# Performance work log

Hardware: AMD Instinct MI355X
Metric: run time of the kernel (lower is better)

Reference implementation:

```python
import jax, jax.numpy as jnp
import numpy as np


def setup_inputs() -> dict:
    key = jax.random.key(0)
    ks = jax.random.split(key, 16)
    B, T, H, E, V = 64, 512, 512, 512, 50257
    sc = 0.02  # weight init scale
    return {
        "enc_seq": jax.random.normal(ks[0], (B, T, H), jnp.float32),
        "enc_mask": jax.random.randint(ks[1], (B, T), 0, 2).astype(jnp.int32),
        "h0": jax.random.normal(ks[2], (1, B, H), jnp.float32),
        "c0": jax.random.normal(ks[3], (1, B, H), jnp.float32),
        "bos_id": 1,
        "eos_id": 2,
        "max_len": 28,
        "emb": jax.random.normal(ks[4], (V, E), jnp.float32) * sc,
        "W_h": jax.random.normal(ks[5], (H, H), jnp.float32) * sc,
        "W_s": jax.random.normal(ks[6], (H, H), jnp.float32) * sc,
        "v": jax.random.normal(ks[7], (H,), jnp.float32) * sc,
        "W_ih": jax.random.normal(ks[8], (4 * H, E + H), jnp.float32) * sc,
        "W_hh": jax.random.normal(ks[9], (4 * H, H), jnp.float32) * sc,
        "b_ih": jnp.zeros((4 * H,), jnp.float32),
        "b_hh": jnp.zeros((4 * H,), jnp.float32),
        "W_out": jax.random.normal(ks[10], (V, H), jnp.float32) * sc,
        "b_out": jnp.zeros((V,), jnp.float32),
    }


def reference(enc_seq, enc_mask, h0, c0, bos_id, eos_id, max_len,
              emb, W_h, W_s, v, W_ih, W_hh, b_ih, b_hh, W_out, b_out):
    B = enc_seq.shape[0]
    h = h0[0]  # [B, H]  (torch: transpose(0,1).squeeze(1))
    c = c0[0]
    # W_h(enc_seq) is loop-invariant; precompute once (same math as per-step recompute)
    Wh_enc = jnp.einsum('bth,kh->btk', enc_seq, W_h)  # [B, T, H]
    neg_inf = jnp.float32(-1e9)
    y0 = jnp.full((B,), bos_id, dtype=jnp.int32)

    def step(carry, _):
        h, c, y = carry
        e_t = emb[y]                                            # [B, E]
        s = h @ W_s.T                                           # [B, H]
        scores = jnp.einsum('bth,h->bt', jnp.tanh(Wh_enc + s[:, None, :]), v)
        scores = jnp.where(enc_mask == 0, neg_inf, scores)
        a = jax.nn.softmax(scores, axis=1)                      # [B, T]
        ctx = jnp.einsum('bt,bth->bh', a, enc_seq)              # [B, H]
        x = jnp.concatenate([e_t, ctx], axis=-1)                # [B, E+H]
        gates = x @ W_ih.T + h @ W_hh.T + b_ih + b_hh           # [B, 4H]
        i, f, g, o = jnp.split(gates, 4, axis=-1)               # torch gate order i,f,g,o
        c2 = jax.nn.sigmoid(f) * c + jax.nn.sigmoid(i) * jnp.tanh(g)
        h2 = jax.nn.sigmoid(o) * jnp.tanh(c2)
        # dropout is identity in eval mode (greedy decoding)
        logits = h2 @ W_out.T + b_out                           # [B, V]
        y2 = jnp.argmax(logits, axis=-1).astype(jnp.int32)
        return (h2, c2, y2), y2

    _, ys = jax.lax.scan(step, (h, c, y0), None, length=max_len - 1)
    return ys.T  # [B, max_len-1] greedy token ids
```

## Files before the change

### kernel.cpp

```cpp
#include <hip/hip_runtime.h>
#include <hip/hip_bf16.h>
#include <cmath>


#define TKK 16

typedef __attribute__((ext_vector_type(8))) short bf16x8;
typedef __attribute__((ext_vector_type(4))) float f32x4;

__device__ inline unsigned short bf16rn(float x) {
  unsigned int u = __float_as_uint(x);
  unsigned int r = u + 0x7fffu + ((u >> 16) & 1u);
  return (unsigned short)(r >> 16);
}
__device__ inline void split1(float x, unsigned short& h, unsigned short& l) {
  h = bf16rn(x);
  float hf = __uint_as_float(((unsigned int)h) << 16);
  l = bf16rn(x - hf);
}

__global__ __launch_bounds__(256) void gemm_tile(
    const float* __restrict__ A, int lda,
    const float* __restrict__ B, int ldb,
    float* __restrict__ C, int ldc,
    int Kchunk, long long c_zstride)
{
  __shared__ __align__(16) float At[TKK][68];
  __shared__ __align__(16) float Bt[TKK][132];
  const int tid = threadIdx.x;
  const int tx = tid & 15, ty = tid >> 4;
  const long long mbase = (long long)blockIdx.y * 64;
  const long long nbase = (long long)blockIdx.x * 128;
  const int kbase = blockIdx.z * Kchunk;
  const float* Ap = A + mbase * lda + kbase;
  const float* Bp = B + nbase * ldb + kbase;
  float acc[4][8];
#pragma unroll
  for (int i = 0; i < 4; i++)
#pragma unroll
    for (int j = 0; j < 8; j++) acc[i][j] = 0.f;

  const int lm = tid >> 2;
  const int lk = (tid & 3) << 2;
  for (int k0 = 0; k0 < Kchunk; k0 += TKK) {
    float4 av = *(const float4*)(Ap + (long long)lm * lda + k0 + lk);
    At[lk + 0][lm] = av.x; At[lk + 1][lm] = av.y;
    At[lk + 2][lm] = av.z; At[lk + 3][lm] = av.w;
#pragma unroll
    for (int r = 0; r < 2; r++) {
      int n = (tid + r * 256) >> 2;
      float4 bv = *(const float4*)(Bp + (long long)n * ldb + k0 + lk);
      Bt[lk + 0][n] = bv.x; Bt[lk + 1][n] = bv.y;
      Bt[lk + 2][n] = bv.z; Bt[lk + 3][n] = bv.w;
    }
    __syncthreads();
#pragma unroll
    for (int kk = 0; kk < TKK; ++kk) {
      float4 a4 = *(const float4*)&At[kk][ty * 4];
      float4 b0 = *(const float4*)&Bt[kk][tx * 4];
      float4 b1 = *(const float4*)&Bt[kk][64 + tx * 4];
      float as[4] = {a4.x, a4.y, a4.z, a4.w};
      float bs[8] = {b0.x, b0.y, b0.z, b0.w, b1.x, b1.y, b1.z, b1.w};
#pragma unroll
      for (int i = 0; i < 4; i++)
#pragma unroll
        for (int j = 0; j < 8; j++)
          acc[i][j] = fmaf(as[i], bs[j], acc[i][j]);
    }
    __syncthreads();
  }
  float* Cp = C + (long long)blockIdx.z * c_zstride;
#pragma unroll
  for (int i = 0; i < 4; i++) {
    long long m = mbase + ty * 4 + i;
    float4 v0, v1;
    v0.x = acc[i][0]; v0.y = acc[i][1]; v0.z = acc[i][2]; v0.w = acc[i][3];
    v1.x = acc[i][4]; v1.y = acc[i][5]; v1.z = acc[i][6]; v1.w = acc[i][7];
    *(float4*)(Cp + m * ldc + nbase + tx * 4) = v0;
    *(float4*)(Cp + m * ldc + nbase + 64 + tx * 4) = v1;
  }
}

__global__ __launch_bounds__(256) void wcat_kernel(
    const float* __restrict__ W_ih, const float* __restrict__ W_hh,
    float* __restrict__ wcat)
{
  long long fi = (long long)blockIdx.x * 256 + threadIdx.x;
  if (fi >= 2048LL * 1536 / 4) return;
  int k = (int)(fi / 384);
  int c = (int)(fi % 384) * 4;
  float4 v;
  if (c < 1024) v = *(const float4*)(W_ih + (long long)k * 1024 + c);
  else          v = *(const float4*)(W_hh + (long long)k * 512 + (c - 1024));
  *(float4*)(wcat + fi * 4) = v;
}

__global__ __launch_bounds__(256) void wcat_split_kernel(
    const float* __restrict__ W_ih, const float* __restrict__ W_hh,
    unsigned short* __restrict__ whi, unsigned short* __restrict__ wlo)
{
  long long fi = (long long)blockIdx.x * 256 + threadIdx.x;
  if (fi >= 2048LL * 1536 / 4) return;
  int k = (int)(fi / 384);
  int c = (int)(fi % 384) * 4;
  float4 v;
  if (c < 1024) v = *(const float4*)(W_ih + (long long)k * 1024 + c);
  else          v = *(const float4*)(W_hh + (long long)k * 512 + (c - 1024));
  long long e = fi * 4;
  float xs[4] = {v.x, v.y, v.z, v.w};
#pragma unroll
  for (int q = 0; q < 4; q++) {
    unsigned short h, l; split1(xs[q], h, l);
    whi[e + q] = h; wlo[e + q] = l;
  }
}

__global__ __launch_bounds__(256) void split_kernel(
    const float* __restrict__ src, unsigned short* __restrict__ hi,
    unsigned short* __restrict__ lo, long long n)
{
  long long i = (long long)blockIdx.x * 256 + threadIdx.x;
  long long stride = (long long)gridDim.x * 256;
  for (long long e = i * 4; e < n; e += stride * 4) {
    float4 v = *(const float4*)(src + e);
    float xs[4] = {v.x, v.y, v.z, v.w};
#pragma unroll
    for (int q = 0; q < 4; q++) {
      unsigned short h, l; split1(xs[q], h, l);
      hi[e + q] = h; lo[e + q] = l;
    }
  }
}

__global__ __launch_bounds__(256) void init_kernel(
    const float* __restrict__ h0, const float* __restrict__ c0,
    const int* __restrict__ bos,
    float* __restrict__ h, float* __restrict__ c, int* __restrict__ y,
    unsigned short* __restrict__ h_hi, unsigned short* __restrict__ h_lo)
{
  int i = blockIdx.x * 256 + threadIdx.x;
  if (i < 64 * 512) {
    float hv = h0[i];
    h[i] = hv; c[i] = c0[i];
    unsigned short hh, hl; split1(hv, hh, hl);
    h_hi[i] = hh; h_lo[i] = hl;
  }
  if (i < 64) y[i] = bos[0];
}

__global__ __launch_bounds__(256) void scores_kernel(
    const float* __restrict__ whenc,
    const float* __restrict__ spart, int np,
    const float* __restrict__ vvec,
    const int* __restrict__ mask,
    float* __restrict__ scores)
{
  const int b = blockIdx.x, tc = blockIdx.y, tid = threadIdx.x;
  __shared__ __align__(16) float sS[512];
  __shared__ __align__(16) float sV[512];
  for (int i = tid; i < 512; i += 256) {
    float s = 0.f;
    for (int p = 0; p < np; ++p) s += spart[(long long)p * 64 * 512 + b * 512 + i];
    sS[i] = s;
    sV[i] = vvec[i];
  }
  __syncthreads();
  const int wave = tid >> 6, lane = tid & 63;
  const int t0 = tc * 128 + wave * 32;
  for (int tt = 0; tt < 32; ++tt) {
    int t = t0 + tt;
    const float* row = whenc + ((long long)b * 512 + t) * 512;
    float p = 0.f;
#pragma unroll
    for (int u = 0; u < 2; ++u) {
      int hb = u * 256 + lane * 4;
      float4 w = *(const float4*)(row + hb);
      float4 s4 = *(const float4*)&sS[hb];
      float4 v4 = *(const float4*)&sV[hb];
      p = fmaf(v4.x, tanhf(w.x + s4.x), p);
      p = fmaf(v4.y, tanhf(w.y + s4.y), p);
      p = fmaf(v4.z, tanhf(w.z + s4.z), p);
      p = fmaf(v4.w, tanhf(w.w + s4.w), p);
    }
#pragma unroll
    for (int off = 32; off; off >>= 1) p += __shfl_xor(p, off);
    if (lane == 0)
      scores[b * 512 + t] = mask[b * 512 + t] ? p : -1e9f;
  }
}

__global__ __launch_bounds__(256) void ctx_kernel(
    const float* __restrict__ scores,
    const float* __restrict__ enc,
    float* __restrict__ ctxp)
{
  const int b = blockIdx.x, tc = blockIdx.y, tid = threadIdx.x;
  __shared__ float sc[512];
  __shared__ float red[256];
  float l0 = scores[b * 512 + tid];
  float l1 = scores[b * 512 + 256 + tid];
  red[tid] = fmaxf(l0, l1);
  __syncthreads();
  for (int s = 128; s > 0; s >>= 1) {
    if (tid < s) red[tid] = fmaxf(red[tid], red[tid + s]);
    __syncthreads();
  }
  float mx = red[0];
  __syncthreads();
  float e0 = expf(l0 - mx), e1 = expf(l1 - mx);
  sc[tid] = e0; sc[tid + 256] = e1;
  red[tid] = e0 + e1;
  __syncthreads();
  for (int s = 128; s > 0; s >>= 1) {
    if (tid < s) red[tid] += red[tid + s];
    __syncthreads();
  }
  float inv = 1.f / red[0];
  float a0 = 0.f, a1 = 0.f;
  for (int u = 0; u < 128; ++u) {
    int t = tc * 128 + u;
    float w = sc[t] * inv;
    const float* row = enc + ((long long)b * 512 + t) * 512;
    float2 e = *(const float2*)(row + tid * 2);
    a0 = fmaf(w, e.x, a0);
    a1 = fmaf(w, e.y, a1);
  }
  float2 o; o.x = a0; o.y = a1;
  *(float2*)(ctxp + ((long long)(b * 4 + tc)) * 512 + tid * 2) = o;
}

__global__ __launch_bounds__(256) void xbuild_kernel(
    const float* __restrict__ emb, const int* __restrict__ y,
    const float* __restrict__ ctxp, const float* __restrict__ h,
    float* __restrict__ xf,
    unsigned short* __restrict__ xhi, unsigned short* __restrict__ xlo)
{
  const int b = blockIdx.x, tid = threadIdx.x;
  const int yb = y[b];
  for (int i = tid; i < 1536; i += 256) {
    float val;
    if (i < 512) {
      val = emb[(long long)yb * 512 + i];
    } else if (i < 1024) {
      int hh = i - 512;
      val = ctxp[(b * 4 + 0) * 512 + hh] + ctxp[(b * 4 + 1) * 512 + hh]
          + ctxp[(b * 4 + 2) * 512 + hh] + ctxp[(b * 4 + 3) * 512 + hh];
    } else {
      val = h[b * 512 + (i - 1024)];
    }
    if (xf) xf[b * 1536 + i] = val;
    if (xhi) {
      unsigned short hh2, ll2; split1(val, hh2, ll2);
      xhi[b * 1536 + i] = hh2; xlo[b * 1536 + i] = ll2;
    }
  }
}

__global__ __launch_bounds__(512) void lstm_kernel(
    const float* __restrict__ gpart, int ngparts,
    const float* __restrict__ b_ih, const float* __restrict__ b_hh,
    float* __restrict__ h, float* __restrict__ c,
    unsigned short* __restrict__ h_hi, unsigned short* __restrict__ h_lo)
{
  const int b = blockIdx.x, hc = threadIdx.x;
  float g[4];
#pragma unroll
  for (int q = 0; q < 4; q++) {
    int k = q * 512 + hc;
    float s = b_ih[k] + b_hh[k];
    for (int p = 0; p < ngparts; ++p)
      s += gpart[((long long)p * 64 + b) * 2048 + k];
    g[q] = s;
  }
  float ig = 1.f / (1.f + expf(-g[0]));
  float fg = 1.f / (1.f + expf(-g[1]));
  float gg = tanhf(g[2]);
  float og = 1.f / (1.f + expf(-g[3]));
  float c2 = fg * c[b * 512 + hc] + ig * gg;
  float h2 = og * tanhf(c2);
  c[b * 512 + hc] = c2;
  h[b * 512 + hc] = h2;
  if (h_hi) {
    unsigned short hh, hl; split1(h2, hh, hl);
    h_hi[b * 512 + hc] = hh; h_lo[b * 512 + hc] = hl;
  }
}

__global__ __launch_bounds__(256) void mfma_gemm(
    const unsigned short* __restrict__ Ahi, const unsigned short* __restrict__ Alo,
    const unsigned short* __restrict__ Bhi, const unsigned short* __restrict__ Blo,
    float* __restrict__ C, int K, int N)
{
  const int tid = threadIdx.x;
  const int w = tid >> 6, l = tid & 63;
  const int arow = blockIdx.y * 64 + w * 16 + (l & 15);
  const int koff = (l >> 4) * 8;
  const int nbase = blockIdx.x * 64;
  f32x4 acc[4];
#pragma unroll
  for (int cf = 0; cf < 4; ++cf) acc[cf] = (f32x4){0.f, 0.f, 0.f, 0.f};

  for (int k0 = 0; k0 < K; k0 += 32) {
    bf16x8 ahi = *(const bf16x8*)(Ahi + (size_t)arow * K + k0 + koff);
    bf16x8 alo = *(const bf16x8*)(Alo + (size_t)arow * K + k0 + koff);
#pragma unroll
    for (int cf = 0; cf < 4; ++cf) {
      int col = nbase + cf * 16 + (l & 15);
      bf16x8 bhi = *(const bf16x8*)(Bhi + (size_t)col * K + k0 + koff);
      bf16x8 blo = *(const bf16x8*)(Blo + (size_t)col * K + k0 + koff);
      acc[cf] = __builtin_amdgcn_mfma_f32_16x16x32_bf16(ahi, bhi, acc[cf], 0, 0, 0);
      acc[cf] = __builtin_amdgcn_mfma_f32_16x16x32_bf16(ahi, blo, acc[cf], 0, 0, 0);
      acc[cf] = __builtin_amdgcn_mfma_f32_16x16x32_bf16(alo, bhi, acc[cf], 0, 0, 0);
    }
  }
#pragma unroll
  for (int cf = 0; cf < 4; ++cf) {
    int col = nbase + cf * 16 + (l & 15);
#pragma unroll
    for (int j = 0; j < 4; ++j) {
      int rowc = blockIdx.y * 64 + w * 16 + (l >> 4) * 4 + j;
      C[(size_t)rowc * N + col] = acc[cf][j];
    }
  }
}

__global__ __launch_bounds__(256) void mfma_logits(
    const unsigned short* __restrict__ Ahi, const unsigned short* __restrict__ Alo,
    const unsigned short* __restrict__ Bhi, const unsigned short* __restrict__ Blo,
    const float* __restrict__ bias, int V, int K,
    float* __restrict__ pval, int* __restrict__ pidx, int nvc)
{
  const int tid = threadIdx.x;
  const int w = tid >> 6, l = tid & 63;
  const int arow = w * 16 + (l & 15);
  const int koff = (l >> 4) * 8;
  const int nbase = blockIdx.x * 64;
  const bf16x8 bz = {0, 0, 0, 0, 0, 0, 0, 0};
  f32x4 acc[4];
#pragma unroll
  for (int cf = 0; cf < 4; ++cf) acc[cf] = (f32x4){0.f, 0.f, 0.f, 0.f};

  for (int k0 = 0; k0 < K; k0 += 32) {
    bf16x8 ahi = *(const bf16x8*)(Ahi + (size_t)arow * K + k0 + koff);
    bf16x8 alo = *(const bf16x8*)(Alo + (size_t)arow * K + k0 + koff);
#pragma unroll
    for (int cf = 0; cf < 4; ++cf) {
      int col = nbase + cf * 16 + (l & 15);
      bf16x8 bhi = bz, blo = bz;
      if (col < V) {
        bhi = *(const bf16x8*)(Bhi + (size_t)col * K + k0 + koff);
        blo = *(const bf16x8*)(Blo + (size_t)col * K + k0 + koff);
      }
      acc[cf] = __builtin_amdgcn_mfma_f32_16x16x32_bf16(ahi, bhi, acc[cf], 0, 0, 0);
      acc[cf] = __builtin_amdgcn_mfma_f32_16x16x32_bf16(ahi, blo, acc[cf], 0, 0, 0);
      acc[cf] = __builtin_amdgcn_mfma_f32_16x16x32_bf16(alo, bhi, acc[cf], 0, 0, 0);
    }
  }
#pragma unroll
  for (int j = 0; j < 4; ++j) {
    float bv = -INFINITY; int bi = 0x7fffffff;
#pragma unroll
    for (int cf = 0; cf < 4; ++cf) {
      int col = nbase + cf * 16 + (l & 15);
      if (col < V) {
        float v = acc[cf][j] + bias[col];
        if (v > bv) { bv = v; bi = col; }
      }
    }
#pragma unroll
    for (int off = 1; off <= 8; off <<= 1) {
      float ov = __shfl_xor(bv, off);
      int oi = __shfl_xor(bi, off);
      if (ov > bv || (ov == bv && oi < bi)) { bv = ov; bi = oi; }
    }
    if ((l & 15) == 0) {
      int b = w * 16 + (l >> 4) * 4 + j;
      pval[b * nvc + blockIdx.x] = bv;
      pidx[b * nvc + blockIdx.x] = bi;
    }
  }
}

__global__ __launch_bounds__(256) void logits_kernel(
    const float* __restrict__ A,
    const float* __restrict__ W,
    const float* __restrict__ bias,
    int V, float* __restrict__ pval, int* __restrict__ pidx, int nvc)
{
  __shared__ __align__(16) float At[TKK][68];
  __shared__ __align__(16) float Bt[TKK][132];
  __shared__ float lv[64][16];
  __shared__ int   li[64][16];
  const int tid = threadIdx.x;
  const int tx = tid & 15, ty = tid >> 4;
  const int nbase = blockIdx.x * 128;
  float acc[4][8];
#pragma unroll
  for (int i = 0; i < 4; i++)
#pragma unroll
    for (int j = 0; j < 8; j++) acc[i][j] = 0.f;
  const int lm = tid >> 2;
  const int lk = (tid & 3) << 2;
  for (int k0 = 0; k0 < 512; k0 += TKK) {
    float4 av = *(const float4*)(A + lm * 512 + k0 + lk);
    At[lk + 0][lm] = av.x; At[lk + 1][lm] = av.y;
    At[lk + 2][lm] = av.z; At[lk + 3][lm] = av.w;
#pragma unroll
    for (int r = 0; r < 2; r++) {
      int n = (tid + r * 256) >> 2;
      int ng = nbase + n;
      float4 bv = make_float4(0.f, 0.f, 0.f, 0.f);
      if (ng < V) bv = *(const float4*)(W + (long long)ng * 512 + k0 + lk);
      Bt[lk + 0][n] = bv.x; Bt[lk + 1][n] = bv.y;
      Bt[lk + 2][n] = bv.z; Bt[lk + 3][n] = bv.w;
    }
    __syncthreads();
#pragma unroll
    for (int kk = 0; kk < TKK; ++kk) {
      float4 a4 = *(const float4*)&At[kk][ty * 4];
      float4 b0 = *(const float4*)&Bt[kk][tx * 4];
      float4 b1 = *(const float4*)&Bt[kk][64 + tx * 4];
      float as[4] = {a4.x, a4.y, a4.z, a4.w};
      float bs[8] = {b0.x, b0.y, b0.z, b0.w, b1.x, b1.y, b1.z, b1.w};
#pragma unroll
      for (int i = 0; i < 4; i++)
#pragma unroll
        for (int j = 0; j < 8; j++)
          acc[i][j] = fmaf(as[i], bs[j], acc[i][j]);
    }
    __syncthreads();
  }
#pragma unroll
  for (int i = 0; i < 4; i++) {
    float bv_ = -INFINITY; int bi_ = 0x7fffffff;
#pragma unroll
    for (int j = 0; j < 8; j++) {
      int vg = (j < 4) ? (nbase + tx * 4 + j) : (nbase + 64 + tx * 4 + (j - 4));
      if (vg < V) {
        float val = acc[i][j] + bias[vg];
        if (val > bv_ || (val == bv_ && vg < bi_)) { bv_ = val; bi_ = vg; }
      }
    }
    lv[ty * 4 + i][tx] = bv_; li[ty * 4 + i][tx] = bi_;
  }
  __syncthreads();
  if (tid < 64) {
    float bv_ = -INFINITY; int bi_ = 0x7fffffff;
#pragma unroll
    for (int t = 0; t < 16; t++) {
      if (lv[tid][t] > bv_ || (lv[tid][t] == bv_ && li[tid][t] < bi_)) {
        bv_ = lv[tid][t]; bi_ = li[tid][t];
      }
    }
    pval[tid * nvc + blockIdx.x] = bv_;
    pidx[tid * nvc + blockIdx.x] = bi_;
  }
}

__global__ __launch_bounds__(64) void argfinal_kernel(
    const float* __restrict__ pval, const int* __restrict__ pidx, int nvc,
    int* __restrict__ y, int* __restrict__ out, int step, int steps)
{
  const int b = blockIdx.x, lane = threadIdx.x;
  float bv = -INFINITY; int bi = 0x7fffffff;
  for (int ci = lane; ci < nvc; ci += 64) {
    float v = pval[b * nvc + ci];
    int ix = pidx[b * nvc + ci];
    if (v > bv || (v == bv && ix < bi)) { bv = v; bi = ix; }
  }
#pragma unroll
  for (int off = 32; off; off >>= 1) {
    float ov = __shfl_xor(bv, off);
    int oi = __shfl_xor(bi, off);
    if (ov > bv || (ov == bv && oi < bi)) { bv = ov; bi = oi; }
  }
  if (lane == 0) { y[b] = bi; out[b * steps + step] = bi; }
}

extern "C" void kernel_launch(void* const* d_in, const int* in_sizes, int n_in,
                              void* d_out, int out_size, void* d_ws, size_t ws_size,
                              hipStream_t stream) {
  const float* enc_seq = (const float*)d_in[0];
  const int*   enc_mask = (const int*)d_in[1];
  const float* h0 = (const float*)d_in[2];
  const float* c0 = (const float*)d_in[3];
  const int*   bos = (const int*)d_in[4];
  const float* emb = (const float*)d_in[7];
  const float* W_h = (const float*)d_in[8];
  const float* W_s = (const float*)d_in[9];
  const float* vvec = (const float*)d_in[10];
  const float* W_ih = (const float*)d_in[11];
  const float* W_hh = (const float*)d_in[12];
  const float* b_ih = (const float*)d_in[13];
  const float* b_hh = (const float*)d_in[14];
  const float* W_out = (const float*)d_in[15];
  const float* b_out = (const float*)d_in[16];

  const int B = 64, T = 512, H = 512;
  const int Vn = in_sizes[15] / 512;
  const int steps = out_size / B;
  int* out = (int*)d_out;

  float* ws = (float*)d_ws;
  size_t off = 0;
  auto alloc = [&](size_t n) { float* p = ws + off; off += (n + 15) & ~(size_t)15; return p; };

  const size_t NEW_NEED = 200ull << 20;
  if (ws_size >= NEW_NEED) {
    const int NVC = (Vn + 63) / 64;
    float* whenc  = alloc((size_t)B * T * H);
    float* sbuf   = alloc((size_t)B * T);
    float* spartf = alloc((size_t)B * H);
    float* ctxp   = alloc((size_t)B * 4 * H);
    float* gbuf   = alloc((size_t)B * 2048);
    float* hbuf   = alloc((size_t)B * H);
    float* cbuf   = alloc((size_t)B * H);
    float* pval   = alloc((size_t)B * NVC);
    int*   pidx   = (int*)alloc((size_t)B * NVC);
    int*   ybuf   = (int*)alloc(B);
    unsigned short* h_hi  = (unsigned short*)alloc((size_t)B * H / 2);
    unsigned short* h_lo  = (unsigned short*)alloc((size_t)B * H / 2);
    unsigned short* x_hi  = (unsigned short*)alloc((size_t)B * 1536 / 2);
    unsigned short* x_lo  = (unsigned short*)alloc((size_t)B * 1536 / 2);
    unsigned short* ws_hi = (unsigned short*)alloc(512ull * 512 / 2);
    unsigned short* ws_lo = (unsigned short*)alloc(512ull * 512 / 2);
    unsigned short* wc_hi = (unsigned short*)alloc(2048ull * 1536 / 2);
    unsigned short* wc_lo = (unsigned short*)alloc(2048ull * 1536 / 2);
    unsigned short* wo_hi = (unsigned short*)alloc((size_t)Vn * 512 / 2);
    unsigned short* wo_lo = (unsigned short*)alloc((size_t)Vn * 512 / 2);

    init_kernel<<<128, 256, 0, stream>>>(h0, c0, bos, hbuf, cbuf, ybuf, h_hi, h_lo);
    wcat_split_kernel<<<3072, 256, 0, stream>>>(W_ih, W_hh, wc_hi, wc_lo);
    split_kernel<<<256, 256, 0, stream>>>(W_s, ws_hi, ws_lo, 512ll * 512);
    split_kernel<<<4096, 256, 0, stream>>>(W_out, wo_hi, wo_lo, (long long)Vn * 512);

    gemm_tile<<<dim3(4, 512, 1), 256, 0, stream>>>(
        enc_seq, 512, W_h, 512, whenc, 512, 512, 0);

    for (int step = 0; step < steps; ++step) {
      mfma_gemm<<<dim3(8, 1), 256, 0, stream>>>(h_hi, h_lo, ws_hi, ws_lo,
                                                spartf, 512, 512);
      scores_kernel<<<dim3(64, 4), 256, 0, stream>>>(whenc, spartf, 1, vvec,
                                                     enc_mask, sbuf);
      ctx_kernel<<<dim3(64, 4), 256, 0, stream>>>(sbuf, enc_seq, ctxp);
      xbuild_kernel<<<64, 256, 0, stream>>>(emb, ybuf, ctxp, hbuf,
                                            nullptr, x_hi, x_lo);
      mfma_gemm<<<dim3(32, 1), 256, 0, stream>>>(x_hi, x_lo, wc_hi, wc_lo,
                                                 gbuf, 1536, 2048);
      lstm_kernel<<<64, 512, 0, stream>>>(gbuf, 1, b_ih, b_hh, hbuf, cbuf,
                                          h_hi, h_lo);
      mfma_logits<<<NVC, 256, 0, stream>>>(h_hi, h_lo, wo_hi, wo_lo, b_out,
                                           Vn, 512, pval, pidx, NVC);
      argfinal_kernel<<<64, 64, 0, stream>>>(pval, pidx, NVC, ybuf, out,
                                             step, steps);
    }
  } else {
    const int NVC = (Vn + 127) / 128;
    float* whenc  = alloc((size_t)B * T * H);
    float* sbuf   = alloc((size_t)B * T);
    float* spart  = alloc(4ull * B * H);
    float* ctxp   = alloc((size_t)B * 4 * H);
    float* xbuf   = alloc((size_t)B * 1536);
    float* gpart  = alloc(3ull * B * 2048);
    float* wcat   = alloc(2048ull * 1536);
    float* hbuf   = alloc((size_t)B * H);
    float* cbuf   = alloc((size_t)B * H);
    float* pval   = alloc((size_t)B * NVC);
    int*   ybuf   = (int*)alloc(B);
    int*   pidx   = (int*)alloc((size_t)B * NVC);
    unsigned short* h_hi = (unsigned short*)alloc((size_t)B * H / 2);
    unsigned short* h_lo = (unsigned short*)alloc((size_t)B * H / 2);

    init_kernel<<<128, 256, 0, stream>>>(h0, c0, bos, hbuf, cbuf, ybuf, h_hi, h_lo);
    wcat_kernel<<<3072, 256, 0, stream>>>(W_ih, W_hh, wcat);
    gemm_tile<<<dim3(4, 512, 1), 256, 0, stream>>>(
        enc_seq, 512, W_h, 512, whenc, 512, 512, 0);

    for (int step = 0; step < steps; ++step) {
      gemm_tile<<<dim3(4, 1, 4), 256, 0, stream>>>(
          hbuf, 512, W_s, 512, spart, 512, 128, (long long)B * H);
      scores_kernel<<<dim3(64, 4), 256, 0, stream>>>(whenc, spart, 4, vvec,
                                                     enc_mask, sbuf);
      ctx_kernel<<<dim3(64, 4), 256, 0, stream>>>(sbuf, enc_seq, ctxp);
      xbuild_kernel<<<64, 256, 0, stream>>>(emb, ybuf, ctxp, hbuf,
                                            xbuf, nullptr, nullptr);
      gemm_tile<<<dim3(16, 1, 3), 256, 0, stream>>>(
          xbuf, 1536, wcat, 1536, gpart, 2048, 512, (long long)B * 2048);
      lstm_kernel<<<64, 512, 0, stream>>>(gpart, 3, b_ih, b_hh, hbuf, cbuf,
                                          nullptr, nullptr);
      logits_kernel<<<NVC, 256, 0, stream>>>(hbuf, W_out, b_out, Vn,
                                             pval, pidx, NVC);
      argfinal_kernel<<<64, 64, 0, stream>>>(pval, pidx, NVC, ybuf, out,
                                             step, steps);
    }
  }
}
```

Measured before the change: 6.973 ms.

## Unify MFMA path, add on-the-fly W_out split fallback, fast tanh, prefetch

The fallback path is removed. The low-workspace case now uses an MFMA logits kernel that splits fp32 W_out into bf16 hi/lo pairs on the fly, so it no longer needs the scalar FMA tiled GEMM. The attention scores kernel replaces tanhf with an exp-plus-reciprocal approximation, trading some accuracy for cheaper transcendentals. mfma_gemm now register double-buffers its global loads to overlap them with MFMA work, and leftover partial-sum reductions and null checks are dropped. The on-the-fly split truncates the hi part instead of rounding it, so results can differ slightly from the precomputed path.

```diff
diff --git a/kernel.cpp b/kernel.cpp
--- a/kernel.cpp
+++ b/kernel.cpp
@@ -17,6 +17,19 @@
   h = bf16rn(x);
   float hf = __uint_as_float(((unsigned int)h) << 16);
   l = bf16rn(x - hf);
+}
+__device__ inline void split_tr(float x, short& h, short& l) {
+  unsigned int u = __float_as_uint(x);
+  h = (short)(u >> 16);
+  float hf = __uint_as_float(u & 0xffff0000u);
+  float d = x - hf;
+  unsigned int ud = __float_as_uint(d);
+  unsigned int r = ud + 0x7fffu + ((ud >> 16) & 1u);
+  l = (short)(r >> 16);
+}
+__device__ inline float tanh_fast(float x) {
+  float e = __expf(2.f * x);
+  return 1.f - 2.f * __builtin_amdgcn_rcpf(e + 1.f);
 }
 
 __global__ __launch_bounds__(256) void gemm_tile(
@@ -81,20 +94,6 @@
   }
 }
 
-__global__ __launch_bounds__(256) void wcat_kernel(
-    const float* __restrict__ W_ih, const float* __restrict__ W_hh,
-    float* __restrict__ wcat)
-{
-  long long fi = (long long)blockIdx.x * 256 + threadIdx.x;
-  if (fi >= 2048LL * 1536 / 4) return;
-  int k = (int)(fi / 384);
-  int c = (int)(fi % 384) * 4;
-  float4 v;
-  if (c < 1024) v = *(const float4*)(W_ih + (long long)k * 1024 + c);
-  else          v = *(const float4*)(W_hh + (long long)k * 512 + (c - 1024));
-  *(float4*)(wcat + fi * 4) = v;
-}
-
 __global__ __launch_bounds__(256) void wcat_split_kernel(
     const float* __restrict__ W_ih, const float* __restrict__ W_hh,
     unsigned short* __restrict__ whi, unsigned short* __restrict__ wlo)
@@ -150,7 +149,7 @@
 
 __global__ __launch_bounds__(256) void scores_kernel(
     const float* __restrict__ whenc,
-    const float* __restrict__ spart, int np,
+    const float* __restrict__ sarr,
     const float* __restrict__ vvec,
     const int* __restrict__ mask,
     float* __restrict__ scores)
@@ -159,9 +158,7 @@
   __shared__ __align__(16) float sS[512];
   __shared__ __align__(16) float sV[512];
   for (int i = tid; i < 512; i += 256) {
-    float s = 0.f;
-    for (int p = 0; p < np; ++p) s += spart[(long long)p * 64 * 512 + b * 512 + i];
-    sS[i] = s;
+    sS[i] = sarr[b * 512 + i];
     sV[i] = vvec[i];
   }
   __syncthreads();
@@ -177,10 +174,10 @@
       float4 w = *(const float4*)(row + hb);
       float4 s4 = *(const float4*)&sS[hb];
       float4 v4 = *(const float4*)&sV[hb];
-      p = fmaf(v4.x, tanhf(w.x + s4.x), p);
-      p = fmaf(v4.y, tanhf(w.y + s4.y), p);
-      p = fmaf(v4.z, tanhf(w.z + s4.z), p);
-      p = fmaf(v4.w, tanhf(w.w + s4.w), p);
+      p = fmaf(v4.x, tanh_fast(w.x + s4.x), p);
+      p = fmaf(v4.y, tanh_fast(w.y + s4.y), p);
+      p = fmaf(v4.z, tanh_fast(w.z + s4.z), p);
+      p = fmaf(v4.w, tanh_fast(w.w + s4.w), p);
     }
 #pragma unroll
     for (int off = 32; off; off >>= 1) p += __shfl_xor(p, off);
@@ -232,7 +229,6 @@
 __global__ __launch_bounds__(256) void xbuild_kernel(
     const float* __restrict__ emb, const int* __restrict__ y,
     const float* __restrict__ ctxp, const float* __restrict__ h,
-    float* __restrict__ xf,
     unsigned short* __restrict__ xhi, unsigned short* __restrict__ xlo)
 {
   const int b = blockIdx.x, tid = threadIdx.x;
@@ -248,16 +244,13 @@
     } else {
       val = h[b * 512 + (i - 1024)];
     }
-    if (xf) xf[b * 1536 + i] = val;
-    if (xhi) {
-      unsigned short hh2, ll2; split1(val, hh2, ll2);
-      xhi[b * 1536 + i] = hh2; xlo[b * 1536 + i] = ll2;
-    }
+    unsigned short hh2, ll2; split1(val, hh2, ll2);
+    xhi[b * 1536 + i] = hh2; xlo[b * 1536 + i] = ll2;
   }
 }
 
 __global__ __launch_bounds__(512) void lstm_kernel(
-    const float* __restrict__ gpart, int ngparts,
+    const float* __restrict__ gates,
     const float* __restrict__ b_ih, const float* __restrict__ b_hh,
     float* __restrict__ h, float* __restrict__ c,
     unsigned short* __restrict__ h_hi, unsigned short* __restrict__ h_lo)
@@ -267,10 +260,7 @@
 #pragma unroll
   for (int q = 0; q < 4; q++) {
     int k = q * 512 + hc;
-    float s = b_ih[k] + b_hh[k];
-    for (int p = 0; p < ngparts; ++p)
-      s += gpart[((long long)p * 64 + b) * 2048 + k];
-    g[q] = s;
+    g[q] = b_ih[k] + b_hh[k] + gates[(long long)b * 2048 + k];
   }
   float ig = 1.f / (1.f + expf(-g[0]));
   float fg = 1.f / (1.f + expf(-g[1]));
@@ -280,10 +270,8 @@
   float h2 = og * tanhf(c2);
   c[b * 512 + hc] = c2;
   h[b * 512 + hc] = h2;
-  if (h_hi) {
-    unsigned short hh, hl; split1(h2, hh, hl);
-    h_hi[b * 512 + hc] = hh; h_lo[b * 512 + hc] = hl;
-  }
+  unsigned short hh, hl; split1(h2, hh, hl);
+  h_hi[b * 512 + hc] = hh; h_lo[b * 512 + hc] = hl;
 }
 
 __global__ __launch_bounds__(256) void mfma_gemm(
@@ -296,22 +284,46 @@
   const int arow = blockIdx.y * 64 + w * 16 + (l & 15);
   const int koff = (l >> 4) * 8;
   const int nbase = blockIdx.x * 64;
+  const size_t aoff = (size_t)arow * K + koff;
+  size_t boff[4];
+#pragma unroll
+  for (int cf = 0; cf < 4; ++cf)
+    boff[cf] = (size_t)(nbase + cf * 16 + (l & 15)) * K + koff;
+
   f32x4 acc[4];
 #pragma unroll
   for (int cf = 0; cf < 4; ++cf) acc[cf] = (f32x4){0.f, 0.f, 0.f, 0.f};
 
+  bf16x8 ah = *(const bf16x8*)(Ahi + aoff);
+  bf16x8 al = *(const bf16x8*)(Alo + aoff);
+  bf16x8 bh[4], bl[4];
+#pragma unroll
+  for (int cf = 0; cf < 4; ++cf) {
+    bh[cf] = *(const bf16x8*)(Bhi + boff[cf]);
+    bl[cf] = *(const bf16x8*)(Blo + boff[cf]);
+  }
   for (int k0 = 0; k0 < K; k0 += 32) {
-    bf16x8 ahi = *(const bf16x8*)(Ahi + (size_t)arow * K + k0 + koff);
-    bf16x8 alo = *(const bf16x8*)(Alo + (size_t)arow * K + k0 + koff);
+    bf16x8 ah2 = ah, al2 = al, bh2[4], bl2[4];
+#pragma unroll
+    for (int cf = 0; cf < 4; ++cf) { bh2[cf] = bh[cf]; bl2[cf] = bl[cf]; }
+    if (k0 + 32 < K) {
+      ah2 = *(const bf16x8*)(Ahi + aoff + k0 + 32);
+      al2 = *(const bf16x8*)(Alo + aoff + k0 + 32);
+#pragma unroll
+      for (int cf = 0; cf < 4; ++cf) {
+        bh2[cf] = *(const bf16x8*)(Bhi + boff[cf] + k0 + 32);
+        bl2[cf] = *(const bf16x8*)(Blo + boff[cf] + k0 + 32);
+      }
+    }
 #pragma unroll
     for (int cf = 0; cf < 4; ++cf) {
-      int col = nbase + cf * 16 + (l & 15);
-      bf16x8 bhi = *(const bf16x8*)(Bhi + (size_t)col * K + k0 + koff);
-      bf16x8 blo = *(const bf16x8*)(Blo + (size_t)col * K + k0 + koff);
-      acc[cf] = __builtin_amdgcn_mfma_f32_16x16x32_bf16(ahi, bhi, acc[cf], 0, 0, 0);
-      acc[cf] = __builtin_amdgcn_mfma_f32_16x16x32_bf16(ahi, blo, acc[cf], 0, 0, 0);
-      acc[cf] = __builtin_amdgcn_mfma_f32_16x16x32_bf16(alo, bhi, acc[cf], 0, 0, 0);
-    }
+      acc[cf] = __builtin_amdgcn_mfma_f32_16x16x32_bf16(ah, bh[cf], acc[cf], 0, 0, 0);
+      acc[cf] = __builtin_amdgcn_mfma_f32_16x16x32_bf16(ah, bl[cf], acc[cf], 0, 0, 0);
+      acc[cf] = __builtin_amdgcn_mfma_f32_16x16x32_bf16(al, bh[cf], acc[cf], 0, 0, 0);
+    }
+    ah = ah2; al = al2;
+#pragma unroll
+    for (int cf = 0; cf < 4; ++cf) { bh[cf] = bh2[cf]; bl[cf] = bl2[cf]; }
   }
 #pragma unroll
   for (int cf = 0; cf < 4; ++cf) {
@@ -324,7 +336,7 @@
   }
 }
 
-__global__ __launch_bounds__(256) void mfma_logits(
+__global__ __launch_bounds__(256) void mfma_logits_pre(
     const unsigned short* __restrict__ Ahi, const unsigned short* __restrict__ Alo,
     const unsigned short* __restrict__ Bhi, const unsigned short* __restrict__ Blo,
     const float* __restrict__ bias, int V, int K,
@@ -381,79 +393,70 @@
   }
 }
 
-__global__ __launch_bounds__(256) void logits_kernel(
-    const float* __restrict__ A,
+__global__ __launch_bounds__(256) void mfma_logits_fly(
+    const unsigned short* __restrict__ Ahi, const unsigned short* __restrict__ Alo,
     const float* __restrict__ W,
-    const float* __restrict__ bias,
-    int V, float* __restrict__ pval, int* __restrict__ pidx, int nvc)
-{
-  __shared__ __align__(16) float At[TKK][68];
-  __shared__ __align__(16) float Bt[TKK][132];
-  __shared__ float lv[64][16];
-  __shared__ int   li[64][16];
+    const float* __restrict__ bias, int V, int K,
+    float* __restrict__ pval, int* __restrict__ pidx, int nvc)
+{
   const int tid = threadIdx.x;
-  const int tx = tid & 15, ty = tid >> 4;
-  const int nbase = blockIdx.x * 128;
-  float acc[4][8];
-#pragma unroll
-  for (int i = 0; i < 4; i++)
-#pragma unroll
-    for (int j = 0; j < 8; j++) acc[i][j] = 0.f;
-  const int lm = tid >> 2;
-  const int lk = (tid & 3) << 2;
-  for (int k0 = 0; k0 < 512; k0 += TKK) {
-    float4 av = *(const float4*)(A + lm * 512 + k0 + lk);
-    At[lk + 0][lm] = av.x; At[lk + 1][lm] = av.y;
-    At[lk + 2][lm] = av.z; At[lk + 3][lm] = av.w;
-#pragma unroll
-    for (int r = 0; r < 2; r++) {
-      int n = (tid + r * 256) >> 2;
-      int ng = nbase + n;
-      float4 bv = make_float4(0.f, 0.f, 0.f, 0.f);
-      if (ng < V) bv = *(const float4*)(W + (long long)ng * 512 + k0 + lk);
-      Bt[lk + 0][n] = bv.x; Bt[lk + 1][n] = bv.y;
-      Bt[lk + 2][n] = bv.z; Bt[lk + 3][n] = bv.w;
-    }
-    __syncthreads();
-#pragma unroll
-    for (int kk = 0; kk < TKK; ++kk) {
-      float4 a4 = *(const float4*)&At[kk][ty * 4];
-      float4 b0 = *(const float4*)&Bt[kk][tx * 4];
-      float4 b1 = *(const float4*)&Bt[kk][64 + tx * 4];
-      float as[4] = {a4.x, a4.y, a4.z, a4.w};
-      float bs[8] = {b0.x, b0.y, b0.z, b0.w, b1.x, b1.y, b1.z, b1.w};
-#pragma unroll
-      for (int i = 0; i < 4; i++)
-#pragma unroll
-        for (int j = 0; j < 8; j++)
-          acc[i][j] = fmaf(as[i], bs[j], acc[i][j]);
-    }
-    __syncthreads();
-  }
-#pragma unroll
-  for (int i = 0; i < 4; i++) {
-    float bv_ = -INFINITY; int bi_ = 0x7fffffff;
-#pragma unroll
-    for (int j = 0; j < 8; j++) {
-      int vg = (j < 4) ? (nbase + tx * 4 + j) : (nbase + 64 + tx * 4 + (j - 4));
-      if (vg < V) {
-        float val = acc[i][j] + bias[vg];
-        if (val > bv_ || (val == bv_ && vg < bi_)) { bv_ = val; bi_ = vg; }
+  const int w = tid >> 6, l = tid & 63;
+  const int arow = w * 16 + (l & 15);
+  const int koff = (l >> 4) * 8;
+  const int nbase = blockIdx.x * 64;
+  const bf16x8 bz = {0, 0, 0, 0, 0, 0, 0, 0};
+  f32x4 acc[4];
+#pragma unroll
+  for (int cf = 0; cf < 4; ++cf) acc[cf] = (f32x4){0.f, 0.f, 0.f, 0.f};
+
+  for (int k0 = 0; k0 < K; k0 += 32) {
+    bf16x8 ahi = *(const bf16x8*)(Ahi + (size_t)arow * K + k0 + koff);
+    bf16x8 alo = *(const bf16x8*)(Alo + (size_t)arow * K + k0 + koff);
+#pragma unroll
+    for (int cf = 0; cf < 4; ++cf) {
+      int col = nbase + cf * 16 + (l & 15);
+      bf16x8 bhi = bz, blo = bz;
+      if (col < V) {
+        const float* wp = W + (size_t)col * K + k0 + koff;
+        float4 fa = *(const float4*)(wp);
+        float4 fb = *(const float4*)(wp + 4);
+        short h_, l_;
+        split_tr(fa.x, h_, l_); bhi[0] = h_; blo[0] = l_;
+        split_tr(fa.y, h_, l_); bhi[1] = h_; blo[1] = l_;
+        split_tr(fa.z, h_, l_); bhi[2] = h_; blo[2] = l_;
+        split_tr(fa.w, h_, l_); bhi[3] = h_; blo[3] = l_;
+        split_tr(fb.x, h_, l_); bhi[4] = h_; blo[4] = l_;
+        split_tr(fb.y, h_, l_); bhi[5] = h_; blo[5] = l_;
+        split_tr(fb.z, h_, l_); bhi[6] = h_; blo[6] = l_;
+        split_tr(fb.w, h_, l_); bhi[7] = h_; blo[7] = l_;
       }
-    }
-    lv[ty * 4 + i][tx] = bv_; li[ty * 4 + i][tx] = bi_;
-  }
-  __syncthreads();
-  if (tid < 64) {
-    float bv_ = -INFINITY; int bi_ = 0x7fffffff;
-#pragma unroll
-    for (int t = 0; t < 16; t++) {
-      if (lv[tid][t] > bv_ || (lv[tid][t] == bv_ && li[tid][t] < bi_)) {
-        bv_ = lv[tid][t]; bi_ = li[tid][t];
+      acc[cf] = __builtin_amdgcn_mfma_f32_16x16x32_bf16(ahi, bhi, acc[cf], 0, 0, 0);
+      acc[cf] = __builtin_amdgcn_mfma_f32_16x16x32_bf16(ahi, blo, acc[cf], 0, 0, 0);
+      acc[cf] = __builtin_amdgcn_mfma_f32_16x16x32_bf16(alo, bhi, acc[cf], 0, 0, 0);
+    }
+  }
+#pragma unroll
+  for (int j = 0; j < 4; ++j) {
+    float bv = -INFINITY; int bi = 0x7fffffff;
+#pragma unroll
+    for (int cf = 0; cf < 4; ++cf) {
+      int col = nbase + cf * 16 + (l & 15);
+      if (col < V) {
+        float v = acc[cf][j] + bias[col];
+        if (v > bv) { bv = v; bi = col; }
       }
     }
-    pval[tid * nvc + blockIdx.x] = bv_;
-    pidx[tid * nvc + blockIdx.x] = bi_;
+#pragma unroll
+    for (int off = 1; off <= 8; off <<= 1) {
+      float ov = __shfl_xor(bv, off);
+      int oi = __shfl_xor(bi, off);
+      if (ov > bv || (ov == bv && oi < bi)) { bv = ov; bi = oi; }
+    }
+    if ((l & 15) == 0) {
+      int b = w * 16 + (l >> 4) * 4 + j;
+      pval[b * nvc + blockIdx.x] = bv;
+      pidx[b * nvc + blockIdx.x] = bi;
+    }
   }
 }
 
@@ -499,99 +502,69 @@
   const int B = 64, T = 512, H = 512;
   const int Vn = in_sizes[15] / 512;
   const int steps = out_size / B;
+  const int NVC = (Vn + 63) / 64;
   int* out = (int*)d_out;
 
   float* ws = (float*)d_ws;
   size_t off = 0;
   auto alloc = [&](size_t n) { float* p = ws + off; off += (n + 15) & ~(size_t)15; return p; };
 
-  const size_t NEW_NEED = 200ull << 20;
-  if (ws_size >= NEW_NEED) {
-    const int NVC = (Vn + 63) / 64;
-    float* whenc  = alloc((size_t)B * T * H);
-    float* sbuf   = alloc((size_t)B * T);
-    float* spartf = alloc((size_t)B * H);
-    float* ctxp   = alloc((size_t)B * 4 * H);
-    float* gbuf   = alloc((size_t)B * 2048);
-    float* hbuf   = alloc((size_t)B * H);
-    float* cbuf   = alloc((size_t)B * H);
-    float* pval   = alloc((size_t)B * NVC);
-    int*   pidx   = (int*)alloc((size_t)B * NVC);
-    int*   ybuf   = (int*)alloc(B);
-    unsigned short* h_hi  = (unsigned short*)alloc((size_t)B * H / 2);
-    unsigned short* h_lo  = (unsigned short*)alloc((size_t)B * H / 2);
-    unsigned short* x_hi  = (unsigned short*)alloc((size_t)B * 1536 / 2);
-    unsigned short* x_lo  = (unsigned short*)alloc((size_t)B * 1536 / 2);
-    unsigned short* ws_hi = (unsigned short*)alloc(512ull * 512 / 2);
-    unsigned short* ws_lo = (unsigned short*)alloc(512ull * 512 / 2);
-    unsigned short* wc_hi = (unsigned short*)alloc(2048ull * 1536 / 2);
-    unsigned short* wc_lo = (unsigned short*)alloc(2048ull * 1536 / 2);
-    unsigned short* wo_hi = (unsigned short*)alloc((size_t)Vn * 512 / 2);
-    unsigned short* wo_lo = (unsigned short*)alloc((size_t)Vn * 512 / 2);
-
-    init_kernel<<<128, 256, 0, stream>>>(h0, c0, bos, hbuf, cbuf, ybuf, h_hi, h_lo);
-    wcat_split_kernel<<<3072, 256, 0, stream>>>(W_ih, W_hh, wc_hi, wc_lo);
-    split_kernel<<<256, 256, 0, stream>>>(W_s, ws_hi, ws_lo, 512ll * 512);
+  float* whenc  = alloc((size_t)B * T * H);
+  float* sbuf   = alloc((size_t)B * T);
+  float* sarr   = alloc((size_t)B * H);
+  float* ctxp   = alloc((size_t)B * 4 * H);
+  float* gbuf   = alloc((size_t)B * 2048);
+  float* hbuf   = alloc((size_t)B * H);
+  float* cbuf   = alloc((size_t)B * H);
+  float* pval   = alloc((size_t)B * NVC);
+  int*   pidx   = (int*)alloc((size_t)B * NVC);
+  int*   ybuf   = (int*)alloc(B);
+  unsigned short* h_hi  = (unsigned short*)alloc((size_t)B * H / 2);
+  unsigned short* h_lo  = (unsigned short*)alloc((size_t)B * H / 2);
+  unsigned short* x_hi  = (unsigned short*)alloc((size_t)B * 1536 / 2);
+  unsigned short* x_lo  = (unsigned short*)alloc((size_t)B * 1536 / 2);
+  unsigned short* ws_hi = (unsigned short*)alloc(512ull * 512 / 2);
+  unsigned short* ws_lo = (unsigned short*)alloc(512ull * 512 / 2);
+  unsigned short* wc_hi = (unsigned short*)alloc(2048ull * 1536 / 2);
+  unsigned short* wc_lo = (unsigned short*)alloc(2048ull * 1536 / 2);
+
+  size_t used = off * sizeof(float);
+  size_t wo_need = (size_t)Vn * 512 * 2 * sizeof(unsigned short) + (1u << 20);
+  bool pre = (ws_size > used) && (ws_size - used >= wo_need);
+  unsigned short* wo_hi = nullptr;
+  unsigned short* wo_lo = nullptr;
+  if (pre) {
+    wo_hi = (unsigned short*)alloc((size_t)Vn * 512 / 2);
+    wo_lo = (unsigned short*)alloc((size_t)Vn * 512 / 2);
+  }
+
+  init_kernel<<<128, 256, 0, stream>>>(h0, c0, bos, hbuf, cbuf, ybuf, h_hi, h_lo);
+  wcat_split_kernel<<<3072, 256, 0, stream>>>(W_ih, W_hh, wc_hi, wc_lo);
+  split_kernel<<<256, 256, 0, stream>>>(W_s, ws_hi, ws_lo, 512ll * 512);
+  if (pre)
     split_kernel<<<4096, 256, 0, stream>>>(W_out, wo_hi, wo_lo, (long long)Vn * 512);
 
-    gemm_tile<<<dim3(4, 512, 1), 256, 0, stream>>>(
-        enc_seq, 512, W_h, 512, whenc, 512, 512, 0);
-
-    for (int step = 0; step < steps; ++step) {
-      mfma_gemm<<<dim3(8, 1), 256, 0, stream>>>(h_hi, h_lo, ws_hi, ws_lo,
-                                                spartf, 512, 512);
-      scores_kernel<<<dim3(64, 4), 256, 0, stream>>>(whenc, spartf, 1, vvec,
-                                                     enc_mask, sbuf);
-      ctx_kernel<<<dim3(64, 4), 256, 0, stream>>>(sbuf, enc_seq, ctxp);
-      xbuild_kernel<<<64, 256, 0, stream>>>(emb, ybuf, ctxp, hbuf,
-                                            nullptr, x_hi, x_lo);
-      mfma_gemm<<<dim3(32, 1), 256, 0, stream>>>(x_hi, x_lo, wc_hi, wc_lo,
-                                                 gbuf, 1536, 2048);
-      lstm_kernel<<<64, 512, 0, stream>>>(gbuf, 1, b_ih, b_hh, hbuf, cbuf,
-                                          h_hi, h_lo);
-      mfma_logits<<<NVC, 256, 0, stream>>>(h_hi, h_lo, wo_hi, wo_lo, b_out,
-                                           Vn, 512, pval, pidx, NVC);
-      argfinal_kernel<<<64, 64, 0, stream>>>(pval, pidx, NVC, ybuf, out,
-                                             step, steps);
-    }
-  } else {
-    const int NVC = (Vn + 127) / 128;
-    float* whenc  = alloc((size_t)B * T * H);
-    float* sbuf   = alloc((size_t)B * T);
-    float* spart  = alloc(4ull * B * H);
-    float* ctxp   = alloc((size_t)B * 4 * H);
-    float* xbuf   = alloc((size_t)B * 1536);
-    float* gpart  = alloc(3ull * B * 2048);
-    float* wcat   = alloc(2048ull * 1536);
-    float* hbuf   = alloc((size_t)B * H);
-    float* cbuf   = alloc((size_t)B * H);
-    float* pval   = alloc((size_t)B * NVC);
-    int*   ybuf   = (int*)alloc(B);
-    int*   pidx   = (int*)alloc((size_t)B * NVC);
-    unsigned short* h_hi = (unsigned short*)alloc((size_t)B * H / 2);
-    unsigned short* h_lo = (unsigned short*)alloc((size_t)B * H / 2);
-
-    init_kernel<<<128, 256, 0, stream>>>(h0, c0, bos, hbuf, cbuf, ybuf, h_hi, h_lo);
-    wcat_kernel<<<3072, 256, 0, stream>>>(W_ih, W_hh, wcat);
-    gemm_tile<<<dim3(4, 512, 1), 256, 0, stream>>>(
-        enc_seq, 512, W_h, 512, whenc, 512, 512, 0);
-
-    for (int step = 0; step < steps; ++step) {
-      gemm_tile<<<dim3(4, 1, 4), 256, 0, stream>>>(
-          hbuf, 512, W_s, 512, spart, 512, 128, (long long)B * H);
-      scores_kernel<<<dim3(64, 4), 256, 0, stream>>>(whenc, spart, 4, vvec,
-                                                     enc_mask, sbuf);
-      ctx_kernel<<<dim3(64, 4), 256, 0, stream>>>(sbuf, enc_seq, ctxp);
-      xbuild_kernel<<<64, 256, 0, stream>>>(emb, ybuf, ctxp, hbuf,
-                                            xbuf, nullptr, nullptr);
-      gemm_tile<<<dim3(16, 1, 3), 256, 0, stream>>>(
-          xbuf, 1536, wcat, 1536, gpart, 2048, 512, (long long)B * 2048);
-      lstm_kernel<<<64, 512, 0, stream>>>(gpart, 3, b_ih, b_hh, hbuf, cbuf,
-                                          nullptr, nullptr);
-      logits_kernel<<<NVC, 256, 0, stream>>>(hbuf, W_out, b_out, Vn,
-                                             pval, pidx, NVC);
-      argfinal_kernel<<<64, 64, 0, stream>>>(pval, pidx, NVC, ybuf, out,
-                                             step, steps);
-    }
-  }
-}
+  gemm_tile<<<dim3(4, 512, 1), 256, 0, stream>>>(
+      enc_seq, 512, W_h, 512, whenc, 512, 512, 0);
+
+  for (int step = 0; step < steps; ++step) {
+    mfma_gemm<<<dim3(8, 1), 256, 0, stream>>>(h_hi, h_lo, ws_hi, ws_lo,
+                                              sarr, 512, 512);
+    scores_kernel<<<dim3(64, 4), 256, 0, stream>>>(whenc, sarr, vvec,
+                                                   enc_mask, sbuf);
+    ctx_kernel<<<dim3(64, 4), 256, 0, stream>>>(sbuf, enc_seq, ctxp);
+    xbuild_kernel<<<64, 256, 0, stream>>>(emb, ybuf, ctxp, hbuf, x_hi, x_lo);
+    mfma_gemm<<<dim3(32, 1), 256, 0, stream>>>(x_hi, x_lo, wc_hi, wc_lo,
+                                               gbuf, 1536, 2048);
+    lstm_kernel<<<64, 512, 0, stream>>>(gbuf, b_ih, b_hh, hbuf, cbuf,
+                                        h_hi, h_lo);
+    if (pre)
+      mfma_logits_pre<<<NVC, 256, 0, stream>>>(h_hi, h_lo, wo_hi, wo_lo, b_out,
+                                               Vn, 512, pval, pidx, NVC);
+    else
+      mfma_logits_fly<<<NVC, 256, 0, stream>>>(h_hi, h_lo, W_out, b_out,
+                                               Vn, 512, pval, pidx, NVC);
+    argfinal_kernel<<<64, 64, 0, stream>>>(pval, pidx, NVC, ybuf, out,
+                                           step, steps);
+  }
+}
```

After: 5.899 ms. 1.18x faster.
